# Kernel tuning notes

Measured on AMD Instinct MI355X. Metric: run time of the kernel, lower is better.

## Reference

```python
import jax, jax.numpy as jnp
import numpy as np
from jax import lax

B, S, D, F, E, K = 4, 2048, 2048, 8192, 8, 2


def setup_inputs() -> dict:
    key = jax.random.key(0)
    ks = jax.random.split(key, 4)
    sd = 1.0 / np.sqrt(D)
    sf = 1.0 / np.sqrt(F)
    return {
        "hidden_states": jax.random.normal(ks[0], (B, S, D), dtype=jnp.float32),
        "router_w": jax.random.normal(ks[1], (D, E), dtype=jnp.float32) * sd,
        "w1": jax.random.normal(ks[2], (E, D, F), dtype=jnp.float32) * sd,
        "b1": jnp.zeros((E, F), dtype=jnp.float32),
        "w2": jax.random.normal(ks[3], (E, F, D), dtype=jnp.float32) * sf,
        "b2": jnp.zeros((E, D), dtype=jnp.float32),
        "top_k": K,
    }


def reference(hidden_states, router_w, w1, b1, w2, b2, top_k):
    b, s, d = hidden_states.shape
    x = hidden_states.reshape(-1, d)  # [T, D] flat tokens
    # Router: top-k over expert logits, softmax over the selected logits.
    logits = x @ router_w                      # [T, E]
    top_vals, top_idx = lax.top_k(logits, top_k)  # [T, K]
    scores = jax.nn.softmax(top_vals, axis=-1)    # [T, K]

    out = jnp.zeros_like(x)
    n_experts = w1.shape[0]
    for e in range(n_experts):  # fixed small expert count
        # per-token combine weight for this expert (0 if not routed)
        cw = jnp.sum(jnp.where(top_idx == e, scores, 0.0), axis=-1)  # [T]
        h = jax.nn.gelu(x @ w1[e] + b1[e], approximate=False)        # [T, F]
        out = out + cw[:, None] * (h @ w2[e] + b2[e])                # masked combine
    out = out.reshape(b, s, d)
    return out + hidden_states  # use_residual=True
```

## Files before the change

kernel.cpp:

```cpp
#include <hip/hip_runtime.h>

#define T_TOK 8192
#define DIM   2048
#define FFN   8192
#define NE    8
#define TOPK  2

typedef unsigned short ushort_t;
typedef unsigned short ushort8  __attribute__((ext_vector_type(8)));
typedef unsigned short ushort4v __attribute__((ext_vector_type(4)));
typedef short bf16x8 __attribute__((ext_vector_type(8)));
typedef float f32x4  __attribute__((ext_vector_type(4)));

__device__ __forceinline__ ushort_t f2bf(float f) {
  unsigned int u = __float_as_uint(f);
  u += 0x7FFFu + ((u >> 16) & 1u);
  return (ushort_t)(u >> 16);
}
__device__ __forceinline__ float bf2f(ushort_t u) {
  return __uint_as_float(((unsigned int)u) << 16);
}

__device__ __forceinline__ void gload16(const void* g, void* l) {
  __builtin_amdgcn_global_load_lds((const __attribute__((address_space(1))) void*)g,
                                   (__attribute__((address_space(3))) void*)l, 16, 0, 0);
}

__device__ __forceinline__ float gelu_exact(float v) {
  float s = v * 0.70710678118654752f;
  float a = fabsf(s);
  float t = __builtin_amdgcn_rcpf(1.0f + 0.3275911f * a);
  float p = t * (0.254829592f +
            t * (-0.284496736f +
            t * (1.421413741f +
            t * (-1.453152027f +
            t * 1.061405429f))));
  float er = 1.0f - p * __expf(-a * a);
  er = copysignf(er, s);
  return 0.5f * v * (1.0f + er);
}

__global__ void k_cast(const float* __restrict__ x, ushort_t* __restrict__ xbf) {
  int i = blockIdx.x * blockDim.x + threadIdx.x;
  float4 v = reinterpret_cast<const float4*>(x)[i];
  ushort4v o;
  o.x = f2bf(v.x); o.y = f2bf(v.y); o.z = f2bf(v.z); o.w = f2bf(v.w);
  reinterpret_cast<ushort4v*>(xbf)[i] = o;
}

#define TT 64
__global__ __launch_bounds__(256) void k_wcvt(const float* __restrict__ in,
                                              ushort_t* __restrict__ outp, int R, int C) {
  __shared__ ushort_t t[TT][TT + 8];
  int e = blockIdx.z;
  const float* src = in + (size_t)e * R * C;
  ushort_t* dst = outp + (size_t)e * R * C;
  int r0 = blockIdx.y * TT, c0 = blockIdx.x * TT;
  int tid = threadIdx.x;
  int rr = tid >> 4;
  int c4 = tid & 15;
#pragma unroll
  for (int i = 0; i < 4; i++) {
    int r = rr + i * 16;
    float4 v = *reinterpret_cast<const float4*>(src + (size_t)(r0 + r) * C + c0 + c4 * 4);
    ushort4v p;
    p.x = f2bf(v.x); p.y = f2bf(v.y); p.z = f2bf(v.z); p.w = f2bf(v.w);
    *reinterpret_cast<ushort4v*>(&t[r][c4 * 4]) = p;
  }
  __syncthreads();
  int c = tid >> 2, rs = tid & 3;
  ushort_t tmp[16];
#pragma unroll
  for (int i = 0; i < 16; i++) tmp[i] = t[rs * 16 + i][c];
  ushort8 v0, v1;
#pragma unroll
  for (int i = 0; i < 8; i++) { v0[i] = tmp[i]; v1[i] = tmp[8 + i]; }
  ushort_t* drow = dst + (size_t)(c0 + c) * R + r0 + rs * 16;
  *reinterpret_cast<ushort8*>(drow) = v0;
  *reinterpret_cast<ushort8*>(drow + 8) = v1;
}

__global__ __launch_bounds__(256) void k_router(
    const float* __restrict__ x, const float* __restrict__ rw,
    int* __restrict__ tidx, float* __restrict__ twt, int* __restrict__ counts) {
  int t = blockIdx.x;
  int tid = threadIdx.x;
  int lane = tid & 63, wave = tid >> 6;
  float acc[NE];
#pragma unroll
  for (int e = 0; e < NE; e++) acc[e] = 0.f;
  const float* xr = x + (size_t)t * DIM;
  for (int d = tid; d < DIM; d += 256) {
    float xv = xr[d];
    const float* r = rw + d * NE;
#pragma unroll
    for (int e = 0; e < NE; e++) acc[e] += xv * r[e];
  }
  __shared__ float wsum[4][NE];
#pragma unroll
  for (int e = 0; e < NE; e++) {
    float v = acc[e];
#pragma unroll
    for (int off = 32; off > 0; off >>= 1) v += __shfl_down(v, off);
    if (lane == 0) wsum[wave][e] = v;
  }
  __syncthreads();
  if (tid == 0) {
    float lg[NE];
#pragma unroll
    for (int e = 0; e < NE; e++) lg[e] = wsum[0][e] + wsum[1][e] + wsum[2][e] + wsum[3][e];
    int i0 = 0; float v0 = lg[0];
#pragma unroll
    for (int e = 1; e < NE; e++) if (lg[e] > v0) { v0 = lg[e]; i0 = e; }
    int i1 = -1; float v1 = -3.4e38f;
#pragma unroll
    for (int e = 0; e < NE; e++) if (e != i0 && lg[e] > v1) { v1 = lg[e]; i1 = e; }
    float e1 = expf(v1 - v0);
    float s = 1.f + e1;
    tidx[t * 2 + 0] = i0; tidx[t * 2 + 1] = i1;
    twt[t * 2 + 0] = 1.f / s; twt[t * 2 + 1] = e1 / s;
    atomicAdd(&counts[i0], 1);
    atomicAdd(&counts[i1], 1);
  }
}

__global__ void k_scan(const int* __restrict__ counts, int* __restrict__ offsets) {
  if (threadIdx.x == 0) {
    int s = 0;
    for (int e = 0; e < NE; e++) { offsets[e] = s; s += counts[e]; }
    offsets[NE] = s;
  }
}

__global__ void k_fill(const int* __restrict__ tidx, const float* __restrict__ twt,
                       const int* __restrict__ offsets, int* __restrict__ cursors,
                       int* __restrict__ ltok, float* __restrict__ lwt, int* __restrict__ ppos) {
  int t = blockIdx.x * blockDim.x + threadIdx.x;
  if (t >= T_TOK) return;
#pragma unroll
  for (int k = 0; k < TOPK; k++) {
    int e = tidx[t * 2 + k];
    int pos = atomicAdd(&cursors[e], 1);
    int p = offsets[e] + pos;
    ltok[p] = t;
    lwt[p] = twt[t * 2 + k];
    ppos[t * 2 + k] = p;
  }
}

#define BM 128
#define BN 128
#define BK 32

__device__ __forceinline__ void xcd_decode(int lin, int nwg, int nx, int& xt, int& yt) {
  int q = nwg >> 3;
  int w = (lin & 7) * q + (lin >> 3);
  xt = w % nx;
  yt = w / nx;
}

__global__ __launch_bounds__(256) void k_gemm1(
    const ushort_t* __restrict__ xbf, const ushort_t* __restrict__ w1t, const float* __restrict__ b1,
    const int* __restrict__ counts, const int* __restrict__ offsets,
    const int* __restrict__ ltok, ushort_t* __restrict__ H) {
  int e = blockIdx.z;
  int cnt = counts[e];
  int xt, yt;
  xcd_decode(blockIdx.x, (T_TOK / BM) * (FFN / BN), T_TOK / BM, xt, yt);
  int row0 = xt * BM;
  if (row0 >= cnt) return;
  int base = offsets[e];
  int col0 = yt * BN;
  const ushort_t* Bt = w1t + (size_t)e * DIM * FFN;

  __shared__ __align__(16) ushort_t As[BM * BK];
  __shared__ __align__(16) ushort_t Bs[BM * BK];

  int tid = threadIdx.x;
  int wave = tid >> 6, lane = tid & 63;
  int wm = wave >> 1, wn = wave & 1;
  int lm = lane & 15, lg = lane >> 4;

  int srow = tid >> 2, seg = tid & 3;
  const ushort_t* asrc[2]; const ushort_t* bsrc[2];
#pragma unroll
  for (int j = 0; j < 2; j++) {
    int ar = min(row0 + j * 64 + srow, cnt - 1);
    asrc[j] = xbf + (size_t)ltok[base + ar] * DIM + seg * 8;
    bsrc[j] = Bt + (size_t)(col0 + j * 64 + srow) * DIM + seg * 8;
  }
  f32x4 acc[4][4];
#pragma unroll
  for (int m = 0; m < 4; m++)
#pragma unroll
    for (int n = 0; n < 4; n++) acc[m][n] = (f32x4){0.f, 0.f, 0.f, 0.f};

  for (int k0 = 0; k0 < DIM; k0 += BK) {
#pragma unroll
    for (int j = 0; j < 2; j++) {
      gload16(asrc[j] + k0, &As[(j * 256 + wave * 64) * 8]);
      gload16(bsrc[j] + k0, &Bs[(j * 256 + wave * 64) * 8]);
    }
    __syncthreads();
    bf16x8 af[4], bfv[4];
#pragma unroll
    for (int m = 0; m < 4; m++)
      af[m] = *reinterpret_cast<const bf16x8*>(&As[(wm * 64 + m * 16 + lm) * BK + lg * 8]);
#pragma unroll
    for (int n = 0; n < 4; n++)
      bfv[n] = *reinterpret_cast<const bf16x8*>(&Bs[(wn * 64 + n * 16 + lm) * BK + lg * 8]);
#pragma unroll
    for (int m = 0; m < 4; m++)
#pragma unroll
      for (int n = 0; n < 4; n++)
        acc[m][n] = __builtin_amdgcn_mfma_f32_16x16x32_bf16(af[m], bfv[n], acc[m][n], 0, 0, 0);
    __syncthreads();
  }
#pragma unroll
  for (int m = 0; m < 4; m++) {
#pragma unroll
    for (int n = 0; n < 4; n++) {
      int f = col0 + wn * 64 + n * 16 + lm;
      float bias = b1[e * FFN + f];
#pragma unroll
      for (int r = 0; r < 4; r++) {
        int row = row0 + wm * 64 + m * 16 + lg * 4 + r;
        if (row < cnt) {
          float v = acc[m][n][r] + bias;
          H[(size_t)(base + row) * FFN + f] = f2bf(gelu_exact(v));
        }
      }
    }
  }
}

__global__ __launch_bounds__(256) void k_gemm2(
    const ushort_t* __restrict__ H, const ushort_t* __restrict__ w2t, const float* __restrict__ b2,
    const int* __restrict__ counts, const int* __restrict__ offsets,
    const float* __restrict__ lwt, ushort_t* __restrict__ contrib) {
  int e = blockIdx.z;
  int cnt = counts[e];
  int xt, yt;
  xcd_decode(blockIdx.x, (T_TOK / BM) * (DIM / BN), T_TOK / BM, xt, yt);
  int row0 = xt * BM;
  if (row0 >= cnt) return;
  int base = offsets[e];
  int col0 = yt * BN;
  const ushort_t* Bt = w2t + (size_t)e * DIM * FFN;

  __shared__ __align__(16) ushort_t As[BM * BK];
  __shared__ __align__(16) ushort_t Bs[BM * BK];

  int tid = threadIdx.x;
  int wave = tid >> 6, lane = tid & 63;
  int wm = wave >> 1, wn = wave & 1;
  int lm = lane & 15, lg = lane >> 4;

  int srow = tid >> 2, seg = tid & 3;
  const ushort_t* asrc[2]; const ushort_t* bsrc[2];
#pragma unroll
  for (int j = 0; j < 2; j++) {
    int ar = min(row0 + j * 64 + srow, cnt - 1);
    asrc[j] = H + (size_t)(base + ar) * FFN + seg * 8;
    bsrc[j] = Bt + (size_t)(col0 + j * 64 + srow) * FFN + seg * 8;
  }
  f32x4 acc[4][4];
#pragma unroll
  for (int m = 0; m < 4; m++)
#pragma unroll
    for (int n = 0; n < 4; n++) acc[m][n] = (f32x4){0.f, 0.f, 0.f, 0.f};

  for (int k0 = 0; k0 < FFN; k0 += BK) {
#pragma unroll
    for (int j = 0; j < 2; j++) {
      gload16(asrc[j] + k0, &As[(j * 256 + wave * 64) * 8]);
      gload16(bsrc[j] + k0, &Bs[(j * 256 + wave * 64) * 8]);
    }
    __syncthreads();
    bf16x8 af[4], bfv[4];
#pragma unroll
    for (int m = 0; m < 4; m++)
      af[m] = *reinterpret_cast<const bf16x8*>(&As[(wm * 64 + m * 16 + lm) * BK + lg * 8]);
#pragma unroll
    for (int n = 0; n < 4; n++)
      bfv[n] = *reinterpret_cast<const bf16x8*>(&Bs[(wn * 64 + n * 16 + lm) * BK + lg * 8]);
#pragma unroll
    for (int m = 0; m < 4; m++)
#pragma unroll
      for (int n = 0; n < 4; n++)
        acc[m][n] = __builtin_amdgcn_mfma_f32_16x16x32_bf16(af[m], bfv[n], acc[m][n], 0, 0, 0);
    __syncthreads();
  }
#pragma unroll
  for (int m = 0; m < 4; m++) {
#pragma unroll
    for (int n = 0; n < 4; n++) {
      int d = col0 + wn * 64 + n * 16 + lm;
      float bias = b2[e * DIM + d];
#pragma unroll
      for (int r = 0; r < 4; r++) {
        int row = row0 + wm * 64 + m * 16 + lg * 4 + r;
        if (row < cnt) {
          float v = (acc[m][n][r] + bias) * lwt[base + row];
          contrib[(size_t)(base + row) * DIM + d] = f2bf(v);
        }
      }
    }
  }
}

__global__ void k_combine(const float* __restrict__ x, const ushort_t* __restrict__ contrib,
                          const int* __restrict__ ppos, float* __restrict__ out) {
  int i = blockIdx.x * blockDim.x + threadIdx.x;
  int t = i / (DIM / 4);
  int dq = i % (DIM / 4);
  int p0 = ppos[t * 2 + 0], p1 = ppos[t * 2 + 1];
  float4 xv = reinterpret_cast<const float4*>(x)[i];
  ushort4v c0 = reinterpret_cast<const ushort4v*>(contrib + (size_t)p0 * DIM)[dq];
  ushort4v c1 = reinterpret_cast<const ushort4v*>(contrib + (size_t)p1 * DIM)[dq];
  float4 o;
  o.x = xv.x + bf2f(c0.x) + bf2f(c1.x);
  o.y = xv.y + bf2f(c0.y) + bf2f(c1.y);
  o.z = xv.z + bf2f(c0.z) + bf2f(c1.z);
  o.w = xv.w + bf2f(c0.w) + bf2f(c1.w);
  reinterpret_cast<float4*>(out)[i] = o;
}

extern "C" void kernel_launch(void* const* d_in, const int* in_sizes, int n_in,
                              void* d_out, int out_size, void* d_ws, size_t ws_size,
                              hipStream_t stream) {
  const float* x  = (const float*)d_in[0];
  const float* rw = (const float*)d_in[1];
  const float* w1 = (const float*)d_in[2];
  const float* b1 = (const float*)d_in[3];
  const float* w2 = (const float*)d_in[4];
  const float* b2 = (const float*)d_in[5];
  float* out = (float*)d_out;
  char* ws = (char*)d_ws;

  const size_t MB = 1u << 20;
  int*   counts  = (int*)(ws);
  int*   offsets = (int*)(ws + 64);
  int*   cursors = (int*)(ws + 128);
  int*   tidx    = (int*)(ws + 1 * MB);
  float* twt     = (float*)(ws + 2 * MB);
  int*   ltok    = (int*)(ws + 3 * MB);
  float* lwt     = (float*)(ws + 4 * MB);
  int*   ppos    = (int*)(ws + 5 * MB);
  ushort_t* xbf     = (ushort_t*)(ws + 8 * MB);
  ushort_t* contrib = (ushort_t*)(ws + 8 * MB);
  ushort_t* Hbuf    = (ushort_t*)(ws + 72 * MB);
  ushort_t* w1t     = (ushort_t*)(ws + 328 * MB);
  ushort_t* w2t     = (ushort_t*)(ws + 328 * MB);
  const size_t NEED = 584 * MB;
  if (ws_size < NEED) {
    hipMemsetAsync(d_out, 0, (size_t)out_size * sizeof(float), stream);
    return;
  }

  hipMemsetAsync(ws, 0, 256, stream);
  k_cast<<<dim3((T_TOK * (size_t)DIM / 4) / 256), 256, 0, stream>>>(x, xbf);
  k_router<<<T_TOK, 256, 0, stream>>>(x, rw, tidx, twt, counts);
  k_scan<<<1, 64, 0, stream>>>(counts, offsets);
  k_fill<<<T_TOK / 256, 256, 0, stream>>>(tidx, twt, offsets, cursors, ltok, lwt, ppos);
  k_wcvt<<<dim3(FFN / TT, DIM / TT, NE), 256, 0, stream>>>(w1, w1t, DIM, FFN);
  k_gemm1<<<dim3((T_TOK / BM) * (FFN / BN), 1, NE), 256, 0, stream>>>(xbf, w1t, b1, counts, offsets, ltok, Hbuf);
  k_wcvt<<<dim3(DIM / TT, FFN / TT, NE), 256, 0, stream>>>(w2, w2t, FFN, DIM);
  k_gemm2<<<dim3((T_TOK / BM) * (DIM / BN), 1, NE), 256, 0, stream>>>(Hbuf, w2t, b2, counts, offsets, lwt, contrib);
  k_combine<<<dim3((T_TOK * (size_t)DIM / 4) / 256), 256, 0, stream>>>(x, contrib, ppos, out);
}
```

Before: 2.187 ms.

## Rewrite expert GEMM1 as 256x256 double-buffered pipelined kernel with swizzled LDS

```diff
diff --git a/kernel.cpp b/kernel.cpp
--- a/kernel.cpp
+++ b/kernel.cpp
@@ -25,6 +25,7 @@
   __builtin_amdgcn_global_load_lds((const __attribute__((address_space(1))) void*)g,
                                    (__attribute__((address_space(3))) void*)l, 16, 0, 0);
 }
+#define SBAR()  { __builtin_amdgcn_sched_barrier(0); __builtin_amdgcn_s_barrier(); __builtin_amdgcn_sched_barrier(0); }
 
 __device__ __forceinline__ float gelu_exact(float v) {
   float s = v * 0.70710678118654752f;
@@ -148,90 +149,149 @@
   }
 }
 
-#define BM 128
-#define BN 128
-#define BK 32
+#define QBM 256
+#define QBN 256
+#define QBK 64
+
+__global__ __launch_bounds__(512, 2) void k_gemm1(
+    const ushort_t* __restrict__ xbf, const ushort_t* __restrict__ w1t, const float* __restrict__ b1,
+    const int* __restrict__ counts, const int* __restrict__ offsets,
+    const int* __restrict__ ltok, ushort_t* __restrict__ H) {
+  int e = blockIdx.z;
+  int cnt = counts[e];
+  int row0 = blockIdx.x * QBM;
+  if (row0 >= cnt) return;
+  int base = offsets[e];
+  int col0 = blockIdx.y * QBN;
+  const ushort_t* Bt = w1t + (size_t)e * DIM * FFN;
+
+  __shared__ __align__(16) ushort_t lds[2][2][2][128 * 64];
+
+  int tid = threadIdx.x;
+  int wid = tid >> 6, lane = tid & 63;
+  int wm = wid >> 2, wn = wid & 3;
+  int lm = lane & 15, lg = lane >> 4;
+  int swz = (lm & 7) * 8;
+
+  const ushort_t* aS[2][2]; const ushort_t* bS[2][2];
+#pragma unroll
+  for (int l = 0; l < 2; l++) {
+    int ch = l * 512 + tid;
+    int rr = ch >> 3;
+    int ss = (ch & 7) ^ (rr & 7);
+#pragma unroll
+    for (int h = 0; h < 2; h++) {
+      int ar = min(row0 + h * 128 + rr, cnt - 1);
+      aS[h][l] = xbf + (size_t)ltok[base + ar] * DIM + ss * 8;
+      bS[h][l] = Bt + (size_t)(col0 + h * 128 + rr) * DIM + ss * 8;
+    }
+  }
+  auto STAGE_A = [&](int b, int k0) {
+#pragma unroll
+    for (int h = 0; h < 2; h++)
+#pragma unroll
+      for (int l = 0; l < 2; l++)
+        gload16(aS[h][l] + k0, &lds[b][0][h][(l * 512 + wid * 64) * 8]);
+  };
+  auto STAGE_B = [&](int b, int h, int k0) {
+#pragma unroll
+    for (int l = 0; l < 2; l++)
+      gload16(bS[h][l] + k0, &lds[b][1][h][(l * 512 + wid * 64) * 8]);
+  };
+
+  f32x4 acc[8][4];
+#pragma unroll
+  for (int m = 0; m < 8; m++)
+#pragma unroll
+    for (int n = 0; n < 4; n++) acc[m][n] = (f32x4){0.f, 0.f, 0.f, 0.f};
+
+  bf16x8 bfr[4][2];
+  auto LD_B = [&](int b) {
+#pragma unroll
+    for (int nf = 0; nf < 4; nf++) {
+      int cI = wn * 64 + nf * 16 + lm;
+      const ushort_t* Bh = &lds[b][1][cI >> 7][(cI & 127) * 64];
+#pragma unroll
+      for (int kk = 0; kk < 2; kk++)
+        bfr[nf][kk] = *reinterpret_cast<const bf16x8*>(&Bh[((kk * 4 + lg) * 8) ^ swz]);
+    }
+  };
+  auto PHASE_A_MM = [&](int b, int q) {
+    bf16x8 af[2][2];
+#pragma unroll
+    for (int mf = 0; mf < 2; mf++) {
+      int rIH = q * 32 + mf * 16 + lm;
+      const ushort_t* Ah = &lds[b][0][wm][rIH * 64];
+#pragma unroll
+      for (int kk = 0; kk < 2; kk++)
+        af[mf][kk] = *reinterpret_cast<const bf16x8*>(&Ah[((kk * 4 + lg) * 8) ^ swz]);
+    }
+    SBAR();
+    __builtin_amdgcn_s_setprio(1);
+#pragma unroll
+    for (int mf = 0; mf < 2; mf++)
+#pragma unroll
+      for (int nf = 0; nf < 4; nf++)
+#pragma unroll
+        for (int kk = 0; kk < 2; kk++)
+          acc[q * 2 + mf][nf] =
+              __builtin_amdgcn_mfma_f32_16x16x32_bf16(af[mf][kk], bfr[nf][kk], acc[q * 2 + mf][nf], 0, 0, 0);
+    __builtin_amdgcn_s_setprio(0);
+  };
+
+  STAGE_A(0, 0);
+  STAGE_B(0, 0, 0); STAGE_B(0, 1, 0);
+  STAGE_B(1, 0, QBK); STAGE_B(1, 1, QBK);
+  asm volatile("s_waitcnt vmcnt(0)" ::: "memory");
+  SBAR();
+
+  const int NT = DIM / QBK;
+  for (int t = 0; t < NT; ++t) {
+    int c = t & 1, o = c ^ 1;
+    int kA = ((t + 1) * QBK) & (DIM - 1);
+    int kB = ((t + 2) * QBK) & (DIM - 1);
+    LD_B(c);
+    STAGE_A(o, kA);
+    PHASE_A_MM(c, 0);
+    SBAR();
+    STAGE_B(c, 0, kB);
+    PHASE_A_MM(c, 1);
+    SBAR();
+    STAGE_B(c, 1, kB);
+    PHASE_A_MM(c, 2);
+    SBAR();
+    PHASE_A_MM(c, 3);
+    asm volatile("s_waitcnt vmcnt(4)" ::: "memory");
+    SBAR();
+  }
+
+#pragma unroll
+  for (int m = 0; m < 8; m++) {
+#pragma unroll
+    for (int n = 0; n < 4; n++) {
+      int f = col0 + wn * 64 + n * 16 + lm;
+      float bias = b1[e * FFN + f];
+#pragma unroll
+      for (int r = 0; r < 4; r++) {
+        int row = row0 + wm * 128 + m * 16 + lg * 4 + r;
+        if (row < cnt) {
+          float v = acc[m][n][r] + bias;
+          H[(size_t)(base + row) * FFN + f] = f2bf(gelu_exact(v));
+        }
+      }
+    }
+  }
+}
+
+#define G2BM 128
+#define G2BN 128
+#define G2BK 32
 
 __device__ __forceinline__ void xcd_decode(int lin, int nwg, int nx, int& xt, int& yt) {
   int q = nwg >> 3;
   int w = (lin & 7) * q + (lin >> 3);
   xt = w % nx;
   yt = w / nx;
-}
-
-__global__ __launch_bounds__(256) void k_gemm1(
-    const ushort_t* __restrict__ xbf, const ushort_t* __restrict__ w1t, const float* __restrict__ b1,
-    const int* __restrict__ counts, const int* __restrict__ offsets,
-    const int* __restrict__ ltok, ushort_t* __restrict__ H) {
-  int e = blockIdx.z;
-  int cnt = counts[e];
-  int xt, yt;
-  xcd_decode(blockIdx.x, (T_TOK / BM) * (FFN / BN), T_TOK / BM, xt, yt);
-  int row0 = xt * BM;
-  if (row0 >= cnt) return;
-  int base = offsets[e];
-  int col0 = yt * BN;
-  const ushort_t* Bt = w1t + (size_t)e * DIM * FFN;
-
-  __shared__ __align__(16) ushort_t As[BM * BK];
-  __shared__ __align__(16) ushort_t Bs[BM * BK];
-
-  int tid = threadIdx.x;
-  int wave = tid >> 6, lane = tid & 63;
-  int wm = wave >> 1, wn = wave & 1;
-  int lm = lane & 15, lg = lane >> 4;
-
-  int srow = tid >> 2, seg = tid & 3;
-  const ushort_t* asrc[2]; const ushort_t* bsrc[2];
-#pragma unroll
-  for (int j = 0; j < 2; j++) {
-    int ar = min(row0 + j * 64 + srow, cnt - 1);
-    asrc[j] = xbf + (size_t)ltok[base + ar] * DIM + seg * 8;
-    bsrc[j] = Bt + (size_t)(col0 + j * 64 + srow) * DIM + seg * 8;
-  }
-  f32x4 acc[4][4];
-#pragma unroll
-  for (int m = 0; m < 4; m++)
-#pragma unroll
-    for (int n = 0; n < 4; n++) acc[m][n] = (f32x4){0.f, 0.f, 0.f, 0.f};
-
-  for (int k0 = 0; k0 < DIM; k0 += BK) {
-#pragma unroll
-    for (int j = 0; j < 2; j++) {
-      gload16(asrc[j] + k0, &As[(j * 256 + wave * 64) * 8]);
-      gload16(bsrc[j] + k0, &Bs[(j * 256 + wave * 64) * 8]);
-    }
-    __syncthreads();
-    bf16x8 af[4], bfv[4];
-#pragma unroll
-    for (int m = 0; m < 4; m++)
-      af[m] = *reinterpret_cast<const bf16x8*>(&As[(wm * 64 + m * 16 + lm) * BK + lg * 8]);
-#pragma unroll
-    for (int n = 0; n < 4; n++)
-      bfv[n] = *reinterpret_cast<const bf16x8*>(&Bs[(wn * 64 + n * 16 + lm) * BK + lg * 8]);
-#pragma unroll
-    for (int m = 0; m < 4; m++)
-#pragma unroll
-      for (int n = 0; n < 4; n++)
-        acc[m][n] = __builtin_amdgcn_mfma_f32_16x16x32_bf16(af[m], bfv[n], acc[m][n], 0, 0, 0);
-    __syncthreads();
-  }
-#pragma unroll
-  for (int m = 0; m < 4; m++) {
-#pragma unroll
-    for (int n = 0; n < 4; n++) {
-      int f = col0 + wn * 64 + n * 16 + lm;
-      float bias = b1[e * FFN + f];
-#pragma unroll
-      for (int r = 0; r < 4; r++) {
-        int row = row0 + wm * 64 + m * 16 + lg * 4 + r;
-        if (row < cnt) {
-          float v = acc[m][n][r] + bias;
-          H[(size_t)(base + row) * FFN + f] = f2bf(gelu_exact(v));
-        }
-      }
-    }
-  }
 }
 
 __global__ __launch_bounds__(256) void k_gemm2(
@@ -241,15 +301,15 @@
   int e = blockIdx.z;
   int cnt = counts[e];
   int xt, yt;
-  xcd_decode(blockIdx.x, (T_TOK / BM) * (DIM / BN), T_TOK / BM, xt, yt);
-  int row0 = xt * BM;
+  xcd_decode(blockIdx.x, (T_TOK / G2BM) * (DIM / G2BN), T_TOK / G2BM, xt, yt);
+  int row0 = xt * G2BM;
   if (row0 >= cnt) return;
   int base = offsets[e];
-  int col0 = yt * BN;
+  int col0 = yt * G2BN;
   const ushort_t* Bt = w2t + (size_t)e * DIM * FFN;
 
-  __shared__ __align__(16) ushort_t As[BM * BK];
-  __shared__ __align__(16) ushort_t Bs[BM * BK];
+  __shared__ __align__(16) ushort_t As[G2BM * G2BK];
+  __shared__ __align__(16) ushort_t Bs[G2BM * G2BK];
 
   int tid = threadIdx.x;
   int wave = tid >> 6, lane = tid & 63;
@@ -270,7 +330,7 @@
 #pragma unroll
     for (int n = 0; n < 4; n++) acc[m][n] = (f32x4){0.f, 0.f, 0.f, 0.f};
 
-  for (int k0 = 0; k0 < FFN; k0 += BK) {
+  for (int k0 = 0; k0 < FFN; k0 += G2BK) {
 #pragma unroll
     for (int j = 0; j < 2; j++) {
       gload16(asrc[j] + k0, &As[(j * 256 + wave * 64) * 8]);
@@ -280,10 +340,10 @@
     bf16x8 af[4], bfv[4];
 #pragma unroll
     for (int m = 0; m < 4; m++)
-      af[m] = *reinterpret_cast<const bf16x8*>(&As[(wm * 64 + m * 16 + lm) * BK + lg * 8]);
+      af[m] = *reinterpret_cast<const bf16x8*>(&As[(wm * 64 + m * 16 + lm) * G2BK + lg * 8]);
 #pragma unroll
     for (int n = 0; n < 4; n++)
-      bfv[n] = *reinterpret_cast<const bf16x8*>(&Bs[(wn * 64 + n * 16 + lm) * BK + lg * 8]);
+      bfv[n] = *reinterpret_cast<const bf16x8*>(&Bs[(wn * 64 + n * 16 + lm) * G2BK + lg * 8]);
 #pragma unroll
     for (int m = 0; m < 4; m++)
 #pragma unroll
@@ -364,8 +424,8 @@
   k_scan<<<1, 64, 0, stream>>>(counts, offsets);
   k_fill<<<T_TOK / 256, 256, 0, stream>>>(tidx, twt, offsets, cursors, ltok, lwt, ppos);
   k_wcvt<<<dim3(FFN / TT, DIM / TT, NE), 256, 0, stream>>>(w1, w1t, DIM, FFN);
-  k_gemm1<<<dim3((T_TOK / BM) * (FFN / BN), 1, NE), 256, 0, stream>>>(xbf, w1t, b1, counts, offsets, ltok, Hbuf);
+  k_gemm1<<<dim3(T_TOK / QBM, FFN / QBN, NE), 512, 0, stream>>>(xbf, w1t, b1, counts, offsets, ltok, Hbuf);
   k_wcvt<<<dim3(DIM / TT, FFN / TT, NE), 256, 0, stream>>>(w2, w2t, FFN, DIM);
-  k_gemm2<<<dim3((T_TOK / BM) * (DIM / BN), 1, NE), 256, 0, stream>>>(Hbuf, w2t, b2, counts, offsets, lwt, contrib);
+  k_gemm2<<<dim3((T_TOK / G2BM) * (DIM / G2BN), 1, NE), 256, 0, stream>>>(Hbuf, w2t, b2, counts, offsets, lwt, contrib);
   k_combine<<<dim3((T_TOK * (size_t)DIM / 4) / 256), 256, 0, stream>>>(x, contrib, ppos, out);
 }
```

Measured after the change: 3.714 ms. 1.7x slower.

## Double-buffer LDS tiles in expert GEMMs with explicit waitcnt pipelining

Applied to the files above, without the earlier changes.

```diff
diff --git a/kernel.cpp b/kernel.cpp
--- a/kernel.cpp
+++ b/kernel.cpp
@@ -24,6 +24,14 @@
 __device__ __forceinline__ void gload16(const void* g, void* l) {
   __builtin_amdgcn_global_load_lds((const __attribute__((address_space(1))) void*)g,
                                    (__attribute__((address_space(3))) void*)l, 16, 0, 0);
+}
+__device__ __forceinline__ unsigned lds_off(const ushort_t* p) {
+  return (unsigned)(uintptr_t)(__attribute__((address_space(3))) const ushort_t*)p;
+}
+__device__ __forceinline__ bf16x8 ds_read128(unsigned off) {
+  bf16x8 r;
+  asm volatile("ds_read_b128 %0, %1" : "=v"(r) : "v"(off));
+  return r;
 }
 
 __device__ __forceinline__ float gelu_exact(float v) {
@@ -151,12 +159,80 @@
 #define BM 128
 #define BN 128
 #define BK 32
+#define BUFB (BM * BK * 2)
 
 __device__ __forceinline__ void xcd_decode(int lin, int nwg, int nx, int& xt, int& yt) {
   int q = nwg >> 3;
   int w = (lin & 7) * q + (lin >> 3);
   xt = w % nx;
   yt = w / nx;
+}
+
+template <int NT>
+__device__ __forceinline__ void gemm_loop(const ushort_t* __restrict__ a0,
+                                          const ushort_t* __restrict__ a1,
+                                          const ushort_t* __restrict__ b0,
+                                          const ushort_t* __restrict__ b1,
+                                          ushort_t* AsLds, ushort_t* BsLds,
+                                          f32x4 (&acc)[4][4]) {
+  int tid = threadIdx.x;
+  int wave = tid >> 6, lane = tid & 63;
+  int wm = wave >> 1, wn = wave & 1;
+  int lm = lane & 15, lg = lane >> 4;
+
+  unsigned abase = lds_off(AsLds), bbase = lds_off(BsLds);
+  unsigned aoff[4], boff[4];
+#pragma unroll
+  for (int m = 0; m < 4; m++)
+    aoff[m] = abase + ((wm * 64 + m * 16 + lm) * BK + lg * 8) * 2;
+#pragma unroll
+  for (int n = 0; n < 4; n++)
+    boff[n] = bbase + ((wn * 64 + n * 16 + lm) * BK + lg * 8) * 2;
+
+  unsigned sdA = (unsigned)((size_t)(wave * 64) * 16);
+  const ushort_t* ap[2] = {a0, a1};
+  const ushort_t* bp[2] = {b0, b1};
+
+  auto STAGE = [&](int buf, int k0) {
+#pragma unroll
+    for (int j = 0; j < 2; j++) {
+      gload16(ap[j] + k0, AsLds + buf * (BM * BK) + (j * 256 + wave * 64) * 8);
+      gload16(bp[j] + k0, BsLds + buf * (BM * BK) + (j * 256 + wave * 64) * 8);
+    }
+  };
+  (void)sdA;
+
+  STAGE(0, 0);
+  int cur = 0;
+  for (int t = 0; t < NT; ++t) {
+    if (t < NT - 1) {
+      STAGE(cur ^ 1, (t + 1) * BK);
+      __builtin_amdgcn_sched_barrier(0);
+      asm volatile("s_waitcnt vmcnt(4)" ::: "memory");
+    } else {
+      __builtin_amdgcn_sched_barrier(0);
+      asm volatile("s_waitcnt vmcnt(0)" ::: "memory");
+    }
+    __builtin_amdgcn_s_barrier();
+    __builtin_amdgcn_sched_barrier(0);
+    unsigned cb = (unsigned)(cur * BUFB);
+    bf16x8 af[4], bv[4];
+#pragma unroll
+    for (int m = 0; m < 4; m++) af[m] = ds_read128(aoff[m] + cb);
+#pragma unroll
+    for (int n = 0; n < 4; n++) bv[n] = ds_read128(boff[n] + cb);
+    asm volatile("s_waitcnt lgkmcnt(0)" ::: "memory");
+    __builtin_amdgcn_sched_barrier(0);
+#pragma unroll
+    for (int m = 0; m < 4; m++)
+#pragma unroll
+      for (int n = 0; n < 4; n++)
+        acc[m][n] = __builtin_amdgcn_mfma_f32_16x16x32_bf16(af[m], bv[n], acc[m][n], 0, 0, 0);
+    __builtin_amdgcn_sched_barrier(0);
+    __builtin_amdgcn_s_barrier();
+    __builtin_amdgcn_sched_barrier(0);
+    cur ^= 1;
+  }
 }
 
 __global__ __launch_bounds__(256) void k_gemm1(
@@ -173,14 +249,10 @@
   int col0 = yt * BN;
   const ushort_t* Bt = w1t + (size_t)e * DIM * FFN;
 
-  __shared__ __align__(16) ushort_t As[BM * BK];
-  __shared__ __align__(16) ushort_t Bs[BM * BK];
+  __shared__ __align__(16) ushort_t As[2 * BM * BK];
+  __shared__ __align__(16) ushort_t Bs[2 * BM * BK];
 
   int tid = threadIdx.x;
-  int wave = tid >> 6, lane = tid & 63;
-  int wm = wave >> 1, wn = wave & 1;
-  int lm = lane & 15, lg = lane >> 4;
-
   int srow = tid >> 2, seg = tid & 3;
   const ushort_t* asrc[2]; const ushort_t* bsrc[2];
 #pragma unroll
@@ -195,27 +267,11 @@
 #pragma unroll
     for (int n = 0; n < 4; n++) acc[m][n] = (f32x4){0.f, 0.f, 0.f, 0.f};
 
-  for (int k0 = 0; k0 < DIM; k0 += BK) {
-#pragma unroll
-    for (int j = 0; j < 2; j++) {
-      gload16(asrc[j] + k0, &As[(j * 256 + wave * 64) * 8]);
-      gload16(bsrc[j] + k0, &Bs[(j * 256 + wave * 64) * 8]);
-    }
-    __syncthreads();
-    bf16x8 af[4], bfv[4];
-#pragma unroll
-    for (int m = 0; m < 4; m++)
-      af[m] = *reinterpret_cast<const bf16x8*>(&As[(wm * 64 + m * 16 + lm) * BK + lg * 8]);
-#pragma unroll
-    for (int n = 0; n < 4; n++)
-      bfv[n] = *reinterpret_cast<const bf16x8*>(&Bs[(wn * 64 + n * 16 + lm) * BK + lg * 8]);
-#pragma unroll
-    for (int m = 0; m < 4; m++)
-#pragma unroll
-      for (int n = 0; n < 4; n++)
-        acc[m][n] = __builtin_amdgcn_mfma_f32_16x16x32_bf16(af[m], bfv[n], acc[m][n], 0, 0, 0);
-    __syncthreads();
-  }
+  gemm_loop<DIM / BK>(asrc[0], asrc[1], bsrc[0], bsrc[1], As, Bs, acc);
+
+  int wave = tid >> 6, lane = tid & 63;
+  int wm = wave >> 1, wn = wave & 1;
+  int lm = lane & 15, lg = lane >> 4;
 #pragma unroll
   for (int m = 0; m < 4; m++) {
 #pragma unroll
@@ -248,14 +304,10 @@
   int col0 = yt * BN;
   const ushort_t* Bt = w2t + (size_t)e * DIM * FFN;
 
-  __shared__ __align__(16) ushort_t As[BM * BK];
-  __shared__ __align__(16) ushort_t Bs[BM * BK];
+  __shared__ __align__(16) ushort_t As[2 * BM * BK];
+  __shared__ __align__(16) ushort_t Bs[2 * BM * BK];
 
   int tid = threadIdx.x;
-  int wave = tid >> 6, lane = tid & 63;
-  int wm = wave >> 1, wn = wave & 1;
-  int lm = lane & 15, lg = lane >> 4;
-
   int srow = tid >> 2, seg = tid & 3;
   const ushort_t* asrc[2]; const ushort_t* bsrc[2];
 #pragma unroll
@@ -270,27 +322,11 @@
 #pragma unroll
     for (int n = 0; n < 4; n++) acc[m][n] = (f32x4){0.f, 0.f, 0.f, 0.f};
 
-  for (int k0 = 0; k0 < FFN; k0 += BK) {
-#pragma unroll
-    for (int j = 0; j < 2; j++) {
-      gload16(asrc[j] + k0, &As[(j * 256 + wave * 64) * 8]);
-      gload16(bsrc[j] + k0, &Bs[(j * 256 + wave * 64) * 8]);
-    }
-    __syncthreads();
-    bf16x8 af[4], bfv[4];
-#pragma unroll
-    for (int m = 0; m < 4; m++)
-      af[m] = *reinterpret_cast<const bf16x8*>(&As[(wm * 64 + m * 16 + lm) * BK + lg * 8]);
-#pragma unroll
-    for (int n = 0; n < 4; n++)
-      bfv[n] = *reinterpret_cast<const bf16x8*>(&Bs[(wn * 64 + n * 16 + lm) * BK + lg * 8]);
-#pragma unroll
-    for (int m = 0; m < 4; m++)
-#pragma unroll
-      for (int n = 0; n < 4; n++)
-        acc[m][n] = __builtin_amdgcn_mfma_f32_16x16x32_bf16(af[m], bfv[n], acc[m][n], 0, 0, 0);
-    __syncthreads();
-  }
+  gemm_loop<FFN / BK>(asrc[0], asrc[1], bsrc[0], bsrc[1], As, Bs, acc);
+
+  int wave = tid >> 6, lane = tid & 63;
+  int wm = wave >> 1, wn = wave & 1;
+  int lm = lane & 15, lg = lane >> 4;
 #pragma unroll
   for (int m = 0; m < 4; m++) {
 #pragma unroll
```

After: 2.385 ms. 9.1% more time.
